# Kernel tuning notes

Measured on AMD Instinct MI355X. Metric: run time of the kernel, lower is better.

The kernel has to match this reference:

```python
import jax, jax.numpy as jnp
import numpy as np

N_FFT = 256
WINDOW_OUT = 64
N_BINS = N_FFT // 2 + 1  # 129


def _irfft_matrices(n_fft, window_out):
    n = n_fft // 2 + 1
    m_real = np.fft.irfft(np.eye(n), n=n_fft)          # [n, n_fft]
    m_imag = np.fft.irfft(1j * np.eye(n), n=n_fft)     # [n, n_fft]
    m_real = m_real[:, -window_out:]                   # truncate to last window_out samples
    m_imag = m_imag[:, -window_out:]
    return (jnp.asarray(m_real, dtype=jnp.float32), jnp.asarray(m_imag, dtype=jnp.float32))


def setup_inputs() -> dict:
    key = jax.random.key(0)
    k1, k2 = jax.random.split(key)
    re = jax.random.normal(k1, (64, 4000, N_BINS), dtype=jnp.float32)
    im = jax.random.normal(k2, (64, 4000, N_BINS), dtype=jnp.float32)
    m_real, m_imag = _irfft_matrices(N_FFT, WINDOW_OUT)
    return {"re": re, "im": im, "m_real": m_real, "m_imag": m_imag}


def reference(re, im, m_real, m_imag):
    # Dense IRFFT: out = re @ M_real + im @ M_imag, fused add of the two matmul outputs.
    # re, im: [B, T, n_bins]; m_real, m_imag: [n_bins, window_out] -> out: [B, T, window_out]
    return jnp.einsum('btn,no->bto', re, m_real) + jnp.einsum('btn,no->bto', im, m_imag)
```

## Files before the change

### kernel.cpp

```cpp
#include <hip/hip_runtime.h>
#include <hip/hip_bf16.h>

typedef __bf16 bf8 __attribute__((ext_vector_type(8)));
typedef float f32x4 __attribute__((ext_vector_type(4)));
typedef unsigned short u16x4 __attribute__((ext_vector_type(4)));

#define NBINS 129
#define ROWS_IT 32
#define ITERS 8
#define KSTR 136
#define MATOFF (ROWS_IT * KSTR)
#define BUFE (2 * MATOFF)

__device__ __forceinline__ unsigned short f2bf(float x) {
    return __builtin_bit_cast(unsigned short, (__bf16)x);
}

__device__ __forceinline__ void issue_loads(const float* __restrict__ re,
                                            const float* __restrict__ im,
                                            int rowbase, int tid,
                                            f32x4* v, float* tl)
{
    #pragma unroll
    for (int j = 0; j < 8; ++j) {
        const int F = tid + j * 256;
        const float* srcp = (j < 4) ? re : im;
        const int row = (F >> 5) & 31;
        const int c   = F & 31;
        __builtin_memcpy(&v[j], srcp + (long)(rowbase + row) * NBINS + c * 4, 16);
    }
    float t = 0.0f;
    if (tid < 64) {
        const float* srcp = (tid < 32) ? re : im;
        t = srcp[(long)(rowbase + (tid & 31)) * NBINS + 128];
    }
    *tl = t;
}

__global__ __launch_bounds__(256, 4)
void irfft_mm(const float* __restrict__ re,
              const float* __restrict__ im,
              const float* __restrict__ mr,
              const float* __restrict__ mi,
              float* __restrict__ out)
{
    __shared__ unsigned short lds[2][BUFE];

    const int tid  = threadIdx.x;
    const int lane = tid & 63;
    const int w    = tid >> 6;
    const int r16  = lane & 15;
    const int q    = lane >> 4;

    const int blockrow = blockIdx.x * (ROWS_IT * ITERS);

    f32x4 v[8]; float tl;
    issue_loads(re, im, blockrow, tid, v, &tl);

    bf8 afr[2][4];
    #pragma unroll
    for (int m = 0; m < 2; ++m) {
        const float* M = m ? mi : mr;
        #pragma unroll
        for (int t = 0; t < 4; ++t) {
            bf8 a;
            #pragma unroll
            for (int j = 0; j < 8; ++j)
                a[j] = (__bf16)M[(t * 32 + q * 8 + j) * 64 + w * 16 + r16];
            afr[m][t] = a;
        }
    }
    const f32x4 mt0 = *(const f32x4*)(mr + 128 * 64 + w * 16 + q * 4);
    const f32x4 mt1 = *(const f32x4*)(mi + 128 * 64 + w * 16 + q * 4);

    for (int it = 0; it < ITERS; ++it) {
        unsigned short* buf = lds[it & 1];
        const int rowbase = blockrow + it * ROWS_IT;

        #pragma unroll
        for (int j = 0; j < 8; ++j) {
            const int F   = tid + j * 256;
            const int mat = j >> 2;
            const int row = (F >> 5) & 31;
            const int c   = F & 31;
            u16x4 h;
            h[0] = f2bf(v[j][0]); h[1] = f2bf(v[j][1]);
            h[2] = f2bf(v[j][2]); h[3] = f2bf(v[j][3]);
            *(u16x4*)&buf[mat * MATOFF + row * KSTR + c * 4] = h;
        }
        if (tid < 64)
            buf[(tid >> 5) * MATOFF + (tid & 31) * KSTR + 128] = f2bf(tl);

        if (it + 1 < ITERS)
            issue_loads(re, im, rowbase + ROWS_IT, tid, v, &tl);

        asm volatile("s_waitcnt lgkmcnt(0)" ::: "memory");
        __builtin_amdgcn_s_barrier();
        asm volatile("" ::: "memory");

        f32x4 acc[2];
        acc[0] = {0.0f, 0.0f, 0.0f, 0.0f};
        acc[1] = {0.0f, 0.0f, 0.0f, 0.0f};

        #pragma unroll
        for (int m = 0; m < 2; ++m) {
            #pragma unroll
            for (int t = 0; t < 4; ++t) {
                bf8 b0 = *(const bf8*)&buf[m * MATOFF + r16 * KSTR + t * 32 + q * 8];
                bf8 b1 = *(const bf8*)&buf[m * MATOFF + (16 + r16) * KSTR + t * 32 + q * 8];
                acc[0] = __builtin_amdgcn_mfma_f32_16x16x32_bf16(afr[m][t], b0, acc[0], 0, 0, 0);
                acc[1] = __builtin_amdgcn_mfma_f32_16x16x32_bf16(afr[m][t], b1, acc[1], 0, 0, 0);
            }
            const f32x4 mt = m ? mt1 : mt0;
            #pragma unroll
            for (int rb = 0; rb < 2; ++rb) {
                const unsigned short h = buf[m * MATOFF + (rb * 16 + r16) * KSTR + 128];
                const float xt = (float)__builtin_bit_cast(__bf16, h);
                #pragma unroll
                for (int jj = 0; jj < 4; ++jj)
                    acc[rb][jj] += xt * mt[jj];
            }
        }

        #pragma unroll
        for (int rb = 0; rb < 2; ++rb)
            *(f32x4*)(out + (long)(rowbase + rb * 16 + r16) * 64 + w * 16 + q * 4) = acc[rb];
    }
}

extern "C" void kernel_launch(void* const* d_in, const int* in_sizes, int n_in,
                              void* d_out, int out_size, void* d_ws, size_t ws_size,
                              hipStream_t stream)
{
    const float* re = (const float*)d_in[0];
    const float* im = (const float*)d_in[1];
    const float* mr = (const float*)d_in[2];
    const float* mi = (const float*)d_in[3];
    float* out = (float*)d_out;

    const long rows = (long)in_sizes[0] / NBINS;
    const int grid = (int)(rows / (ROWS_IT * ITERS));
    irfft_mm<<<grid, 256, 0, stream>>>(re, im, mr, mi, out);
}
```

Baseline: 67.87 us.

## Deepen global-load prefetch to two iterations and use nontemporal output stores

```diff
diff --git a/kernel.cpp b/kernel.cpp
--- a/kernel.cpp
+++ b/kernel.cpp
@@ -18,21 +18,21 @@
 
 __device__ __forceinline__ void issue_loads(const float* __restrict__ re,
                                             const float* __restrict__ im,
-                                            int rowbase, int tid,
+                                            int rowbase, int myrow, int mycol, int tid,
                                             f32x4* v, float* tl)
 {
     #pragma unroll
-    for (int j = 0; j < 8; ++j) {
-        const int F = tid + j * 256;
-        const float* srcp = (j < 4) ? re : im;
-        const int row = (F >> 5) & 31;
-        const int c   = F & 31;
-        __builtin_memcpy(&v[j], srcp + (long)(rowbase + row) * NBINS + c * 4, 16);
+    for (int m = 0; m < 2; ++m) {
+        const float* srcp = m ? im : re;
+        #pragma unroll
+        for (int jj = 0; jj < 4; ++jj)
+            __builtin_memcpy(&v[m * 4 + jj],
+                             srcp + (rowbase + myrow + jj * 8) * NBINS + mycol * 4, 16);
     }
     float t = 0.0f;
     if (tid < 64) {
         const float* srcp = (tid < 32) ? re : im;
-        t = srcp[(long)(rowbase + (tid & 31)) * NBINS + 128];
+        t = srcp[(rowbase + (tid & 31)) * NBINS + 128];
     }
     *tl = t;
 }
@@ -46,16 +46,20 @@
 {
     __shared__ unsigned short lds[2][BUFE];
 
-    const int tid  = threadIdx.x;
-    const int lane = tid & 63;
-    const int w    = tid >> 6;
-    const int r16  = lane & 15;
-    const int q    = lane >> 4;
+    const int tid   = threadIdx.x;
+    const int lane  = tid & 63;
+    const int w     = tid >> 6;
+    const int r16   = lane & 15;
+    const int q     = lane >> 4;
+    const int myrow = tid >> 5;
+    const int mycol = tid & 31;
 
     const int blockrow = blockIdx.x * (ROWS_IT * ITERS);
 
-    f32x4 v[8]; float tl;
-    issue_loads(re, im, blockrow, tid, v, &tl);
+    f32x4 v[2][8];
+    float tl[2];
+    issue_loads(re, im, blockrow,           myrow, mycol, tid, v[0], &tl[0]);
+    issue_loads(re, im, blockrow + ROWS_IT, myrow, mycol, tid, v[1], &tl[1]);
 
     bf8 afr[2][4];
     #pragma unroll
@@ -73,34 +77,35 @@
     const f32x4 mt0 = *(const f32x4*)(mr + 128 * 64 + w * 16 + q * 4);
     const f32x4 mt1 = *(const f32x4*)(mi + 128 * 64 + w * 16 + q * 4);
 
+    #pragma unroll
     for (int it = 0; it < ITERS; ++it) {
         unsigned short* buf = lds[it & 1];
         const int rowbase = blockrow + it * ROWS_IT;
+        f32x4* vc = v[it & 1];
 
         #pragma unroll
-        for (int j = 0; j < 8; ++j) {
-            const int F   = tid + j * 256;
-            const int mat = j >> 2;
-            const int row = (F >> 5) & 31;
-            const int c   = F & 31;
-            u16x4 h;
-            h[0] = f2bf(v[j][0]); h[1] = f2bf(v[j][1]);
-            h[2] = f2bf(v[j][2]); h[3] = f2bf(v[j][3]);
-            *(u16x4*)&buf[mat * MATOFF + row * KSTR + c * 4] = h;
-        }
+        for (int m = 0; m < 2; ++m)
+            #pragma unroll
+            for (int jj = 0; jj < 4; ++jj) {
+                const f32x4 x = vc[m * 4 + jj];
+                u16x4 h;
+                h[0] = f2bf(x[0]); h[1] = f2bf(x[1]);
+                h[2] = f2bf(x[2]); h[3] = f2bf(x[3]);
+                *(u16x4*)&buf[m * MATOFF + (myrow + jj * 8) * KSTR + mycol * 4] = h;
+            }
         if (tid < 64)
-            buf[(tid >> 5) * MATOFF + (tid & 31) * KSTR + 128] = f2bf(tl);
+            buf[(tid >> 5) * MATOFF + (tid & 31) * KSTR + 128] = f2bf(tl[it & 1]);
 
-        if (it + 1 < ITERS)
-            issue_loads(re, im, rowbase + ROWS_IT, tid, v, &tl);
+        if (it + 2 < ITERS)
+            issue_loads(re, im, rowbase + 2 * ROWS_IT, myrow, mycol, tid,
+                        vc, &tl[it & 1]);
 
         asm volatile("s_waitcnt lgkmcnt(0)" ::: "memory");
         __builtin_amdgcn_s_barrier();
         asm volatile("" ::: "memory");
 
-        f32x4 acc[2];
-        acc[0] = {0.0f, 0.0f, 0.0f, 0.0f};
-        acc[1] = {0.0f, 0.0f, 0.0f, 0.0f};
+        f32x4 acc0 = {0.0f, 0.0f, 0.0f, 0.0f};
+        f32x4 acc1 = {0.0f, 0.0f, 0.0f, 0.0f};
 
         #pragma unroll
         for (int m = 0; m < 2; ++m) {
@@ -108,23 +113,25 @@
             for (int t = 0; t < 4; ++t) {
                 bf8 b0 = *(const bf8*)&buf[m * MATOFF + r16 * KSTR + t * 32 + q * 8];
                 bf8 b1 = *(const bf8*)&buf[m * MATOFF + (16 + r16) * KSTR + t * 32 + q * 8];
-                acc[0] = __builtin_amdgcn_mfma_f32_16x16x32_bf16(afr[m][t], b0, acc[0], 0, 0, 0);
-                acc[1] = __builtin_amdgcn_mfma_f32_16x16x32_bf16(afr[m][t], b1, acc[1], 0, 0, 0);
+                acc0 = __builtin_amdgcn_mfma_f32_16x16x32_bf16(afr[m][t], b0, acc0, 0, 0, 0);
+                acc1 = __builtin_amdgcn_mfma_f32_16x16x32_bf16(afr[m][t], b1, acc1, 0, 0, 0);
             }
             const f32x4 mt = m ? mt1 : mt0;
+            const float x0 =
+                (float)__builtin_bit_cast(__bf16, buf[m * MATOFF + r16 * KSTR + 128]);
+            const float x1 =
+                (float)__builtin_bit_cast(__bf16, buf[m * MATOFF + (16 + r16) * KSTR + 128]);
             #pragma unroll
-            for (int rb = 0; rb < 2; ++rb) {
-                const unsigned short h = buf[m * MATOFF + (rb * 16 + r16) * KSTR + 128];
-                const float xt = (float)__builtin_bit_cast(__bf16, h);
-                #pragma unroll
-                for (int jj = 0; jj < 4; ++jj)
-                    acc[rb][jj] += xt * mt[jj];
+            for (int jj = 0; jj < 4; ++jj) {
+                acc0[jj] += x0 * mt[jj];
+                acc1[jj] += x1 * mt[jj];
             }
         }
 
-        #pragma unroll
-        for (int rb = 0; rb < 2; ++rb)
-            *(f32x4*)(out + (long)(rowbase + rb * 16 + r16) * 64 + w * 16 + q * 4) = acc[rb];
+        __builtin_nontemporal_store(
+            acc0, (f32x4*)(out + (rowbase + r16) * 64 + w * 16 + q * 4));
+        __builtin_nontemporal_store(
+            acc1, (f32x4*)(out + (rowbase + 16 + r16) * 64 + w * 16 + q * 4));
     }
 }
 
```

Result: slower. 104.8 us (+54.4%).

## Stream fp32 inputs directly to LDS via global_load_lds with XOR swizzle

Applied to the files above, without the earlier changes.

```diff
diff --git a/kernel.cpp b/kernel.cpp
--- a/kernel.cpp
+++ b/kernel.cpp
@@ -3,38 +3,17 @@
 
 typedef __bf16 bf8 __attribute__((ext_vector_type(8)));
 typedef float f32x4 __attribute__((ext_vector_type(4)));
-typedef unsigned short u16x4 __attribute__((ext_vector_type(4)));
 
 #define NBINS 129
-#define ROWS_IT 32
-#define ITERS 8
-#define KSTR 136
-#define MATOFF (ROWS_IT * KSTR)
-#define BUFE (2 * MATOFF)
+#define ROWS_IT 16
+#define ITERS 16
+#define MATB 8192
+#define BUFB (2 * MATB)
 
-__device__ __forceinline__ unsigned short f2bf(float x) {
-    return __builtin_bit_cast(unsigned short, (__bf16)x);
-}
-
-__device__ __forceinline__ void issue_loads(const float* __restrict__ re,
-                                            const float* __restrict__ im,
-                                            int rowbase, int tid,
-                                            f32x4* v, float* tl)
-{
-    #pragma unroll
-    for (int j = 0; j < 8; ++j) {
-        const int F = tid + j * 256;
-        const float* srcp = (j < 4) ? re : im;
-        const int row = (F >> 5) & 31;
-        const int c   = F & 31;
-        __builtin_memcpy(&v[j], srcp + (long)(rowbase + row) * NBINS + c * 4, 16);
-    }
-    float t = 0.0f;
-    if (tid < 64) {
-        const float* srcp = (tid < 32) ? re : im;
-        t = srcp[(long)(rowbase + (tid & 31)) * NBINS + 128];
-    }
-    *tl = t;
+__device__ __forceinline__ void gload_lds16(const float* src, char* ldsdst) {
+    __builtin_amdgcn_global_load_lds(
+        (const __attribute__((address_space(1))) void*)src,
+        (__attribute__((address_space(3))) void*)ldsdst, 16, 0, 0);
 }
 
 __global__ __launch_bounds__(256, 4)
@@ -44,18 +23,37 @@
               const float* __restrict__ mi,
               float* __restrict__ out)
 {
-    __shared__ unsigned short lds[2][BUFE];
+    __shared__ __align__(16) char lds[2][BUFB];
 
     const int tid  = threadIdx.x;
     const int lane = tid & 63;
     const int w    = tid >> 6;
     const int r16  = lane & 15;
     const int q    = lane >> 4;
+    const int rk   = r16 & 7;
 
     const int blockrow = blockIdx.x * (ROWS_IT * ITERS);
 
-    f32x4 v[8]; float tl;
-    issue_loads(re, im, blockrow, tid, v, &tl);
+    const int    smat  = w >> 1;
+    const int    srow0 = (w & 1) * 8;
+    const float* ssrc  = smat ? im : re;
+    const int    lrow  = lane >> 5;
+    const int    p     = lane & 31;
+
+    float trr[2], tri[2];
+
+    {
+        char* b0 = lds[0];
+        #pragma unroll
+        for (int i = 0; i < 4; ++i) {
+            const int trow = srow0 + 2 * i + lrow;
+            const int g    = p ^ (trow & 7);
+            gload_lds16(ssrc + (long)(blockrow + trow) * NBINS + g * 4,
+                        b0 + smat * MATB + (srow0 + 2 * i) * 512 + lane * 16);
+        }
+        trr[0] = re[(long)(blockrow + r16) * NBINS + 128];
+        tri[0] = im[(long)(blockrow + r16) * NBINS + 128];
+    }
 
     bf8 afr[2][4];
     #pragma unroll
@@ -73,58 +71,60 @@
     const f32x4 mt0 = *(const f32x4*)(mr + 128 * 64 + w * 16 + q * 4);
     const f32x4 mt1 = *(const f32x4*)(mi + 128 * 64 + w * 16 + q * 4);
 
+    #pragma unroll
     for (int it = 0; it < ITERS; ++it) {
-        unsigned short* buf = lds[it & 1];
+        char* bufc = lds[it & 1];
         const int rowbase = blockrow + it * ROWS_IT;
 
-        #pragma unroll
-        for (int j = 0; j < 8; ++j) {
-            const int F   = tid + j * 256;
-            const int mat = j >> 2;
-            const int row = (F >> 5) & 31;
-            const int c   = F & 31;
-            u16x4 h;
-            h[0] = f2bf(v[j][0]); h[1] = f2bf(v[j][1]);
-            h[2] = f2bf(v[j][2]); h[3] = f2bf(v[j][3]);
-            *(u16x4*)&buf[mat * MATOFF + row * KSTR + c * 4] = h;
+        if (it + 1 < ITERS) {
+            char* bn = lds[(it + 1) & 1];
+            const int rbn = rowbase + ROWS_IT;
+            #pragma unroll
+            for (int i = 0; i < 4; ++i) {
+                const int trow = srow0 + 2 * i + lrow;
+                const int g    = p ^ (trow & 7);
+                gload_lds16(ssrc + (long)(rbn + trow) * NBINS + g * 4,
+                            bn + smat * MATB + (srow0 + 2 * i) * 512 + lane * 16);
+            }
+            trr[(it + 1) & 1] = re[(long)(rbn + r16) * NBINS + 128];
+            tri[(it + 1) & 1] = im[(long)(rbn + r16) * NBINS + 128];
         }
-        if (tid < 64)
-            buf[(tid >> 5) * MATOFF + (tid & 31) * KSTR + 128] = f2bf(tl);
 
-        if (it + 1 < ITERS)
-            issue_loads(re, im, rowbase + ROWS_IT, tid, v, &tl);
+        __builtin_amdgcn_sched_barrier(0);
+        if (it + 1 < ITERS) asm volatile("s_waitcnt vmcnt(6)" ::: "memory");
+        else                asm volatile("s_waitcnt vmcnt(1)" ::: "memory");
+        __builtin_amdgcn_s_barrier();
+        __builtin_amdgcn_sched_barrier(0);
 
-        asm volatile("s_waitcnt lgkmcnt(0)" ::: "memory");
-        __builtin_amdgcn_s_barrier();
-        asm volatile("" ::: "memory");
-
-        f32x4 acc[2];
-        acc[0] = {0.0f, 0.0f, 0.0f, 0.0f};
-        acc[1] = {0.0f, 0.0f, 0.0f, 0.0f};
-
+        f32x4 acc = {0.0f, 0.0f, 0.0f, 0.0f};
         #pragma unroll
         for (int m = 0; m < 2; ++m) {
+            const char* mb = bufc + m * MATB + r16 * 512;
             #pragma unroll
             for (int t = 0; t < 4; ++t) {
-                bf8 b0 = *(const bf8*)&buf[m * MATOFF + r16 * KSTR + t * 32 + q * 8];
-                bf8 b1 = *(const bf8*)&buf[m * MATOFF + (16 + r16) * KSTR + t * 32 + q * 8];
-                acc[0] = __builtin_amdgcn_mfma_f32_16x16x32_bf16(afr[m][t], b0, acc[0], 0, 0, 0);
-                acc[1] = __builtin_amdgcn_mfma_f32_16x16x32_bf16(afr[m][t], b1, acc[1], 0, 0, 0);
+                const int j0 = t * 8 + q * 2;
+                const f32x4 lo = *(const f32x4*)(mb + ((j0)     ^ rk) * 16);
+                const f32x4 hi = *(const f32x4*)(mb + ((j0 + 1) ^ rk) * 16);
+                bf8 bfr;
+                #pragma unroll
+                for (int jj = 0; jj < 4; ++jj) {
+                    bfr[jj]     = (__bf16)lo[jj];
+                    bfr[4 + jj] = (__bf16)hi[jj];
+                }
+                acc = __builtin_amdgcn_mfma_f32_16x16x32_bf16(afr[m][t], bfr, acc, 0, 0, 0);
             }
+            const float xt = m ? tri[it & 1] : trr[it & 1];
             const f32x4 mt = m ? mt1 : mt0;
             #pragma unroll
-            for (int rb = 0; rb < 2; ++rb) {
-                const unsigned short h = buf[m * MATOFF + (rb * 16 + r16) * KSTR + 128];
-                const float xt = (float)__builtin_bit_cast(__bf16, h);
-                #pragma unroll
-                for (int jj = 0; jj < 4; ++jj)
-                    acc[rb][jj] += xt * mt[jj];
-            }
+            for (int jj = 0; jj < 4; ++jj) acc[jj] += xt * mt[jj];
         }
 
-        #pragma unroll
-        for (int rb = 0; rb < 2; ++rb)
-            *(f32x4*)(out + (long)(rowbase + rb * 16 + r16) * 64 + w * 16 + q * 4) = acc[rb];
+        *(f32x4*)(out + (long)(rowbase + r16) * 64 + w * 16 + q * 4) = acc;
+
+        if (it + 1 < ITERS) {
+            __builtin_amdgcn_sched_barrier(0);
+            __builtin_amdgcn_s_barrier();
+        }
     }
 }
 
```

Result: slower. 69.59 us (+2.5%).
